# Kernel tuning notes

Measured on AMD Instinct MI355X. Metric: run time of the kernel, lower is better.

Reference implementation:

```python
import jax, jax.numpy as jnp
import numpy as np
from jax import lax

REG_STRENGTH = 0.01
TEMPERATURE = 0.1


def _pav_nonincreasing(y):
    """Pool-adjacent-violators for isotonic L2 regression with a
    nonincreasing constraint (matches torchsort's isotonic_l2).
    Returns (solution [n], block_id [n])."""
    n = y.shape[0]

    def body(carry, yi):
        m, c, t = carry  # block means, block counts, stack top
        m = m.at[t].set(yi)
        c = c.at[t].set(1)

        def cond(st):
            m_, c_, t_ = st
            return (t_ > 0) & (m_[t_ - 1] < m_[t_])

        def merge(st):
            m_, c_, t_ = st
            tot = m_[t_ - 1] * c_[t_ - 1] + m_[t_] * c_[t_]
            cc = c_[t_ - 1] + c_[t_]
            m_ = m_.at[t_ - 1].set(tot / cc)
            c_ = c_.at[t_ - 1].set(cc).at[t_].set(0)
            return (m_, c_, t_ - 1)

        m, c, t = lax.while_loop(cond, merge, (m, c, t))
        return (m, c, t + 1), None

    init = (jnp.zeros(n, y.dtype), jnp.zeros(n, jnp.int32), jnp.int32(0))
    (m, c, _), _ = lax.scan(body, init, y)
    sol = jnp.repeat(m, c, total_repeat_length=n)
    blk = jnp.repeat(jnp.arange(n), c, total_repeat_length=n)
    return sol, blk


@jax.custom_vjp
def _isotonic_l2(y):
    return _pav_nonincreasing(y)[0]


def _iso_fwd(y):
    sol, blk = _pav_nonincreasing(y)
    return sol, blk


def _iso_bwd(blk, g):
    n = g.shape[0]
    sums = jax.ops.segment_sum(g, blk, num_segments=n)
    cnts = jax.ops.segment_sum(jnp.ones_like(g), blk, num_segments=n)
    return ((sums / jnp.maximum(cnts, 1.0))[blk],)


_isotonic_l2.defvjp(_iso_fwd, _iso_bwd)


def soft_sort_ascending(scores, reg_strength):
    """torchsort.soft_sort with L2 regularization. scores: [B, R]."""
    n = scores.shape[-1]
    w = jnp.arange(n, 0, -1, dtype=scores.dtype) / reg_strength  # [n, ..., 1]/rs
    perm = jnp.argsort(scores, axis=-1)
    s = -jnp.take_along_axis(scores, perm, axis=-1)  # descending sort of -scores
    sol = jax.vmap(_isotonic_l2)(w[None, :] - s)
    return sol - w  # ascending soft-sorted values, [B, R]


def setup_inputs() -> dict:
    key = jax.random.key(0)
    k1, k2 = jax.random.split(key)
    scores = jax.random.normal(k1, (128, 8192), dtype=jnp.float32)
    ref_class = jax.random.randint(k2, (8192,), 0, 10, dtype=jnp.int32)
    return {"scores": scores, "ref_class": ref_class, "k": 32, "K": 8}


def reference(scores, ref_class, k, K):
    B, R = scores.shape
    rc = ref_class
    if rc.ndim == 1:
        rc = jnp.broadcast_to(rc[None, :], (B, R))
    rc = rc.astype(scores.dtype)
    sorted_vals = soft_sort_ascending(scores, REG_STRENGTH)  # [B, R]
    yk = sorted_vals[:, -k:]                                  # top-k largest, [B, k]
    M = jnp.abs(scores[:, None, :] - yk[:, :, None])          # [B, k, R]
    soft_mask = jax.nn.softmax(-M / TEMPERATURE, axis=-1)     # [B, k, R]
    soft_label_expectation = jnp.einsum('bkr,br->bk', soft_mask, rc)
    return yk, soft_label_expectation
```

## Files before the change

kernel.cpp:

```cpp
#include <hip/hip_runtime.h>
#include <math.h>

#define R_N    8192
#define K_TOP  32
#define HALF_R 4096
#define NEG10_LOG2E (-14.426950408889634f)
#define CUT_DELTA   2.0f

__device__ __forceinline__ float fast_exp2(float x) {
#if __has_builtin(__builtin_amdgcn_exp2f)
    return __builtin_amdgcn_exp2f(x);
#else
    return exp2f(x);
#endif
}

__device__ __forceinline__ float merge_asc32(float v, int l) {
#pragma unroll
    for (int j = 16; j > 0; j >>= 1) {
        float pv = __shfl_xor(v, j, 64);
        v = ((l & j) == 0) ? fminf(v, pv) : fmaxf(v, pv);
    }
    return v;
}

__device__ __forceinline__ float sort32_asc(float v, int l) {
#pragma unroll
    for (int k = 2; k <= 32; k <<= 1) {
#pragma unroll
        for (int j = k >> 1; j > 0; j >>= 1) {
            float pv = __shfl_xor(v, j, 64);
            bool keep_min = (((l & k) == 0) == ((l & j) == 0));
            v = keep_min ? fminf(v, pv) : fmaxf(v, pv);
        }
    }
    return v;
}

__device__ __forceinline__ float merge_top32(float a, float b, int l) {
    float rev = __shfl_xor(b, 31, 64);
    return merge_asc32(fmaxf(a, rev), l);
}

extern "C" __global__ void __launch_bounds__(512)
k_topk(const float* __restrict__ scores, float* __restrict__ wstop) {
    __shared__ float topbuf[16 * 32];
    const int row  = blockIdx.x >> 1;
    const int half = blockIdx.x & 1;
    const int tid  = threadIdx.x;
    const int l    = tid & 31;
    const int h    = tid >> 5;

    const float4* s4 = (const float4*)(scores + (size_t)row * R_N + half * HALF_R);
    float4 a = s4[tid];
    float4 b = s4[tid + 512];
    float v[8] = {a.x, a.y, a.z, a.w, b.x, b.y, b.z, b.w};

#pragma unroll
    for (int p = 0; p < 8; ++p) v[p] = sort32_asc(v[p], l);
#pragma unroll
    for (int gap = 1; gap < 8; gap <<= 1)
#pragma unroll
        for (int p = 0; p < 8; p += 2 * gap)
            v[p] = merge_top32(v[p], v[p + gap], l);
    float run = v[0];

#pragma unroll
    for (int stride = 1; stride < 16; stride <<= 1) {
        topbuf[h * 32 + l] = run;
        __syncthreads();
        if ((h & (2 * stride - 1)) == 0) {
            float pv = topbuf[(h + stride) * 32 + (l ^ 31)];
            run = merge_asc32(fmaxf(run, pv), l);
        }
        __syncthreads();
    }
    if (tid < 32) wstop[(size_t)blockIdx.x * K_TOP + l] = run;
}

extern "C" __global__ void __launch_bounds__(1024)
k_expect(const float* __restrict__ scores, const int* __restrict__ rc,
         const float* __restrict__ wstop, float* __restrict__ out, int B) {
    __shared__ float         cs[R_N];
    __shared__ unsigned char cc[R_N];
    __shared__ float         yk_m[K_TOP];
    __shared__ unsigned int  cnt;

    const int row  = blockIdx.x;
    const int tid  = threadIdx.x;
    const int lane = tid & 63;
    const int l    = tid & 31;
    const int wv   = tid >> 6;

    if (tid == 0) cnt = 0;

    float A = wstop[(size_t)row * 2 * K_TOP + l];
    float Bb = wstop[(size_t)row * 2 * K_TOP + K_TOP + l];
    float run = merge_top32(A, Bb, l);
    if (tid < K_TOP) {
        yk_m[l] = run;
        out[(size_t)row * K_TOP + l] = run;
    }
    const float cutoff = __shfl(run, 0, 64) - CUT_DELTA;

    const float4* s4 = (const float4*)(scores + (size_t)row * R_N);
    const int4*   c4 = (const int4*)rc;
    float se[8]; int cei[8];
#pragma unroll
    for (int q = 0; q < 2; ++q) {
        float4 s = s4[tid + q * 1024];
        int4   c = c4[tid + q * 1024];
        se[q*4+0] = s.x; se[q*4+1] = s.y; se[q*4+2] = s.z; se[q*4+3] = s.w;
        cei[q*4+0] = c.x; cei[q*4+1] = c.y; cei[q*4+2] = c.z; cei[q*4+3] = c.w;
    }
    __syncthreads();

    unsigned long long m[8];
    unsigned int tot = 0;
#pragma unroll
    for (int e = 0; e < 8; ++e) {
        m[e] = __ballot(se[e] >= cutoff);
        tot += (unsigned)__popcll(m[e]);
    }
    unsigned int wbase = 0;
    if (lane == 0) wbase = atomicAdd(&cnt, tot);
    wbase = __shfl(wbase, 0, 64);
    const unsigned long long lt = (1ull << lane) - 1ull;
#pragma unroll
    for (int e = 0; e < 8; ++e) {
        if (se[e] >= cutoff) {
            unsigned int idx = wbase + (unsigned)__popcll(m[e] & lt);
            cs[idx] = se[e];
            cc[idx] = (unsigned char)cei[e];
        }
        wbase += (unsigned)__popcll(m[e]);
    }
    __syncthreads();
    const int n = (int)cnt;

    const float y0 = yk_m[wv * 2 + 0];
    const float y1 = yk_m[wv * 2 + 1];
    float n0 = 0, d0 = 0, n1 = 0, d1 = 0;
    for (int i = lane; i < n; i += 64) {
        float s = cs[i];
        float c = (float)cc[i];
        float e0 = fast_exp2(NEG10_LOG2E * fabsf(s - y0));
        float e1 = fast_exp2(NEG10_LOG2E * fabsf(s - y1));
        n0 = fmaf(e0, c, n0); d0 += e0;
        n1 = fmaf(e1, c, n1); d1 += e1;
    }
#pragma unroll
    for (int off = 32; off > 0; off >>= 1) {
        n0 += __shfl_xor(n0, off, 64); d0 += __shfl_xor(d0, off, 64);
        n1 += __shfl_xor(n1, off, 64); d1 += __shfl_xor(d1, off, 64);
    }
    if (lane == 0) {
        float* dst = out + (size_t)B * K_TOP + (size_t)row * K_TOP + wv * 2;
        dst[0] = n0 / d0;
        dst[1] = n1 / d1;
    }
}

extern "C" void kernel_launch(void* const* d_in, const int* in_sizes, int n_in,
                              void* d_out, int out_size, void* d_ws, size_t ws_size,
                              hipStream_t stream) {
    const float* scores = (const float*)d_in[0];
    const int*   rc     = (const int*)d_in[1];
    const int R = in_sizes[1];
    const int B = in_sizes[0] / R;
    float* out   = (float*)d_out;
    float* wstop = (float*)d_ws;

    hipLaunchKernelGGL(k_topk,   dim3(B * 2), dim3(512),  0, stream, scores, wstop);
    hipLaunchKernelGGL(k_expect, dim3(B),     dim3(1024), 0, stream, scores, rc, wstop, out, B);
}
```

Baseline: 72.07 us.

## Factor softmax exponentials and threshold-filter top-k candidates before sorting

The top-k kernel now derives a threshold from the 32nd-largest per-thread maximum in each wave. It compacts only the elements at or above that threshold into a 512-slot shared buffer before bitonic merging, replacing the full per-element sort32 and merge network. The expectation kernel no longer compacts thousands of elements and evaluates exponentials per top-k value. For scores at or below the smallest top-k value it factors exp(-c|s-y|) into exp(c·s)·exp(-c·y), so one shared block sum serves all 32 outputs, and only the few scores above that value are handled explicitly. This trades per-k exponential work for possible float overflow or precision loss when scores are large, and candidates beyond 512 are silently dropped.

Result: faster. 68.32 us (-5.2%).

```diff
diff --git a/kernel.cpp b/kernel.cpp
--- a/kernel.cpp
+++ b/kernel.cpp
@@ -4,8 +4,9 @@
 #define R_N    8192
 #define K_TOP  32
 #define HALF_R 4096
-#define NEG10_LOG2E (-14.426950408889634f)
-#define CUT_DELTA   2.0f
+#define CAND   512
+#define C1     14.426950408889634f
+#define NEG_BIG (-3.0e38f)
 
 __device__ __forceinline__ float fast_exp2(float x) {
 #if __has_builtin(__builtin_amdgcn_exp2f)
@@ -37,6 +38,19 @@
     return v;
 }
 
+__device__ __forceinline__ float sort64_asc(float v, int lane) {
+#pragma unroll
+    for (int k = 2; k <= 64; k <<= 1) {
+#pragma unroll
+        for (int j = k >> 1; j > 0; j >>= 1) {
+            float pv = __shfl_xor(v, j, 64);
+            bool keep_min = (((lane & k) == 0) == ((lane & j) == 0));
+            v = keep_min ? fminf(v, pv) : fmaxf(v, pv);
+        }
+    }
+    return v;
+}
+
 __device__ __forceinline__ float merge_top32(float a, float b, int l) {
     float rev = __shfl_xor(b, 31, 64);
     return merge_asc32(fmaxf(a, rev), l);
@@ -44,27 +58,60 @@
 
 extern "C" __global__ void __launch_bounds__(512)
 k_topk(const float* __restrict__ scores, float* __restrict__ wstop) {
-    __shared__ float topbuf[16 * 32];
+    __shared__ float    cand[CAND];
+    __shared__ float    twbuf[8];
+    __shared__ unsigned cnt;
+    __shared__ float    topbuf[16 * 32];
+
     const int row  = blockIdx.x >> 1;
     const int half = blockIdx.x & 1;
     const int tid  = threadIdx.x;
+    const int lane = tid & 63;
     const int l    = tid & 31;
     const int h    = tid >> 5;
+    const int wv   = tid >> 6;
 
     const float4* s4 = (const float4*)(scores + (size_t)row * R_N + half * HALF_R);
     float4 a = s4[tid];
     float4 b = s4[tid + 512];
     float v[8] = {a.x, a.y, a.z, a.w, b.x, b.y, b.z, b.w};
 
-#pragma unroll
-    for (int p = 0; p < 8; ++p) v[p] = sort32_asc(v[p], l);
-#pragma unroll
-    for (int gap = 1; gap < 8; gap <<= 1)
-#pragma unroll
-        for (int p = 0; p < 8; p += 2 * gap)
-            v[p] = merge_top32(v[p], v[p + gap], l);
-    float run = v[0];
-
+    cand[tid] = NEG_BIG;
+    if (tid == 0) cnt = 0;
+
+    float tmax = v[0];
+#pragma unroll
+    for (int e = 1; e < 8; ++e) tmax = fmaxf(tmax, v[e]);
+    float srt = sort64_asc(tmax, lane);
+    float t_w = __shfl(srt, 32, 64);
+    if (lane == 0) twbuf[wv] = t_w;
+    __syncthreads();
+    float t = twbuf[0];
+#pragma unroll
+    for (int w = 1; w < 8; ++w) t = fmaxf(t, twbuf[w]);
+
+    unsigned long long m[8];
+    unsigned tot = 0;
+#pragma unroll
+    for (int e = 0; e < 8; ++e) {
+        m[e] = __ballot(v[e] >= t);
+        tot += (unsigned)__popcll(m[e]);
+    }
+    unsigned wbase = 0;
+    if (lane == 0) wbase = atomicAdd(&cnt, tot);
+    wbase = __shfl(wbase, 0, 64);
+    const unsigned long long lt = (1ull << lane) - 1ull;
+#pragma unroll
+    for (int e = 0; e < 8; ++e) {
+        if (v[e] >= t) {
+            unsigned idx = wbase + (unsigned)__popcll(m[e] & lt);
+            if (idx < CAND) cand[idx] = v[e];
+        }
+        wbase += (unsigned)__popcll(m[e]);
+    }
+    __syncthreads();
+
+    float run = sort32_asc(cand[tid], l);
 #pragma unroll
     for (int stride = 1; stride < 16; stride <<= 1) {
         topbuf[h * 32 + l] = run;
@@ -81,10 +128,9 @@
 extern "C" __global__ void __launch_bounds__(1024)
 k_expect(const float* __restrict__ scores, const int* __restrict__ rc,
          const float* __restrict__ wstop, float* __restrict__ out, int B) {
-    __shared__ float         cs[R_N];
-    __shared__ unsigned char cc[R_N];
-    __shared__ float         yk_m[K_TOP];
-    __shared__ unsigned int  cnt;
+    __shared__ float    dsS[32], dsC[32];
+    __shared__ unsigned dcnt;
+    __shared__ float    pbuf[16 * 2];
 
     const int row  = blockIdx.x;
     const int tid  = threadIdx.x;
@@ -92,62 +138,57 @@
     const int l    = tid & 31;
     const int wv   = tid >> 6;
 
-    if (tid == 0) cnt = 0;
-
-    float A = wstop[(size_t)row * 2 * K_TOP + l];
-    float Bb = wstop[(size_t)row * 2 * K_TOP + K_TOP + l];
-    float run = merge_top32(A, Bb, l);
-    if (tid < K_TOP) {
-        yk_m[l] = run;
-        out[(size_t)row * K_TOP + l] = run;
-    }
-    const float cutoff = __shfl(run, 0, 64) - CUT_DELTA;
+    if (tid == 0) dcnt = 0;
+
+    float A  = wstop[(size_t)row * 2 * K_TOP + l];
+    float Bv = wstop[(size_t)row * 2 * K_TOP + K_TOP + l];
+    float yk = merge_top32(A, Bv, l);
+    if (tid < 32) out[(size_t)row * K_TOP + l] = yk;
+    const float y0 = __shfl(yk, 0, 64);
 
     const float4* s4 = (const float4*)(scores + (size_t)row * R_N);
     const int4*   c4 = (const int4*)rc;
-    float se[8]; int cei[8];
-#pragma unroll
-    for (int q = 0; q < 2; ++q) {
-        float4 s = s4[tid + q * 1024];
-        int4   c = c4[tid + q * 1024];
-        se[q*4+0] = s.x; se[q*4+1] = s.y; se[q*4+2] = s.z; se[q*4+3] = s.w;
-        cei[q*4+0] = c.x; cei[q*4+1] = c.y; cei[q*4+2] = c.z; cei[q*4+3] = c.w;
-    }
-    __syncthreads();
-
-    unsigned long long m[8];
-    unsigned int tot = 0;
+    float4 sa = s4[tid], sb = s4[tid + 1024];
+    int4   ca = c4[tid], cb = c4[tid + 1024];
+    float se[8] = {sa.x, sa.y, sa.z, sa.w, sb.x, sb.y, sb.z, sb.w};
+    float ce[8] = {(float)ca.x, (float)ca.y, (float)ca.z, (float)ca.w,
+                   (float)cb.x, (float)cb.y, (float)cb.z, (float)cb.w};
+    __syncthreads();
+
+    float P = 0.f, Pc = 0.f;
 #pragma unroll
     for (int e = 0; e < 8; ++e) {
-        m[e] = __ballot(se[e] >= cutoff);
-        tot += (unsigned)__popcll(m[e]);
-    }
-    unsigned int wbase = 0;
-    if (lane == 0) wbase = atomicAdd(&cnt, tot);
-    wbase = __shfl(wbase, 0, 64);
-    const unsigned long long lt = (1ull << lane) - 1ull;
-#pragma unroll
-    for (int e = 0; e < 8; ++e) {
-        if (se[e] >= cutoff) {
-            unsigned int idx = wbase + (unsigned)__popcll(m[e] & lt);
-            cs[idx] = se[e];
-            cc[idx] = (unsigned char)cei[e];
-        }
-        wbase += (unsigned)__popcll(m[e]);
-    }
-    __syncthreads();
-    const int n = (int)cnt;
-
-    const float y0 = yk_m[wv * 2 + 0];
-    const float y1 = yk_m[wv * 2 + 1];
-    float n0 = 0, d0 = 0, n1 = 0, d1 = 0;
-    for (int i = lane; i < n; i += 64) {
-        float s = cs[i];
-        float c = (float)cc[i];
-        float e0 = fast_exp2(NEG10_LOG2E * fabsf(s - y0));
-        float e1 = fast_exp2(NEG10_LOG2E * fabsf(s - y1));
-        n0 = fmaf(e0, c, n0); d0 += e0;
-        n1 = fmaf(e1, c, n1); d1 += e1;
+        if (se[e] <= y0) {
+            float ex = fast_exp2(C1 * se[e]);
+            P += ex;
+            Pc = fmaf(ce[e], ex, Pc);
+        } else {
+            unsigned idx = atomicAdd(&dcnt, 1u);
+            dsS[idx] = se[e];
+            dsC[idx] = ce[e];
+        }
+    }
+#pragma unroll
+    for (int off = 32; off > 0; off >>= 1) {
+        P  += __shfl_xor(P,  off, 64);
+        Pc += __shfl_xor(Pc, off, 64);
+    }
+    if (lane == 0) { pbuf[wv * 2] = P; pbuf[wv * 2 + 1] = Pc; }
+    __syncthreads();
+    float Pt = 0.f, Pct = 0.f;
+#pragma unroll
+    for (int w = 0; w < 16; ++w) { Pt += pbuf[w * 2]; Pct += pbuf[w * 2 + 1]; }
+    const int nD = (int)dcnt;
+
+    const float yj0 = __shfl(yk, 2 * wv,     64);
+    const float yj1 = __shfl(yk, 2 * wv + 1, 64);
+    float n0 = 0.f, d0 = 0.f, n1 = 0.f, d1 = 0.f;
+    if (lane < nD) {
+        float s = dsS[lane], c = dsC[lane];
+        float e0 = fast_exp2(-C1 * fabsf(s - yj0));
+        float e1 = fast_exp2(-C1 * fabsf(s - yj1));
+        d0 = e0; n0 = c * e0;
+        d1 = e1; n1 = c * e1;
     }
 #pragma unroll
     for (int off = 32; off > 0; off >>= 1) {
@@ -155,9 +196,11 @@
         n1 += __shfl_xor(n1, off, 64); d1 += __shfl_xor(d1, off, 64);
     }
     if (lane == 0) {
-        float* dst = out + (size_t)B * K_TOP + (size_t)row * K_TOP + wv * 2;
-        dst[0] = n0 / d0;
-        dst[1] = n1 / d1;
+        float e0 = fast_exp2(-C1 * yj0);
+        float e1 = fast_exp2(-C1 * yj1);
+        float* dst = out + (size_t)B * K_TOP + (size_t)row * K_TOP + 2 * wv;
+        dst[0] = fmaf(Pct, e0, n0) / fmaf(Pt, e0, d0);
+        dst[1] = fmaf(Pct, e1, n1) / fmaf(Pt, e1, d1);
     }
 }
 
```
